# Optimization experiments

Hardware: AMD Instinct MI355X
Metric: run time of the kernel (lower is better)

Reference implementation:

```python
import jax, jax.numpy as jnp
import numpy as np

D_MODEL = 1024
N_HEADS = 16
N_GROUPS = 4
HEAD_DIM = D_MODEL // N_HEADS          # 64
HPG = N_HEADS // N_GROUPS              # heads per group = 4
KV_DIM = N_GROUPS * HEAD_DIM           # 256


def setup_inputs() -> dict:
    key = jax.random.key(0)
    ks = jax.random.split(key, 9)
    B, T = 2, 2048
    s = 0.02
    return {
        "x":  jax.random.normal(ks[0], (B, T, D_MODEL), dtype=jnp.float32),
        "Wq": jax.random.normal(ks[1], (D_MODEL, D_MODEL), dtype=jnp.float32) * s,
        "bq": jnp.zeros((D_MODEL,), dtype=jnp.float32),
        "Wk": jax.random.normal(ks[2], (D_MODEL, KV_DIM), dtype=jnp.float32) * s,
        "bk": jnp.zeros((KV_DIM,), dtype=jnp.float32),
        "Wv": jax.random.normal(ks[3], (D_MODEL, KV_DIM), dtype=jnp.float32) * s,
        "bv": jnp.zeros((KV_DIM,), dtype=jnp.float32),
        "Wo": jax.random.normal(ks[4], (D_MODEL, D_MODEL), dtype=jnp.float32) * s,
        "bo": jnp.zeros((D_MODEL,), dtype=jnp.float32),
    }


def reference(x, Wq, bq, Wk, bk, Wv, bv, Wo, bo):
    B, T, C = x.shape
    q = x @ Wq + bq                                   # [B,T,C]
    k = x @ Wk + bk                                   # [B,T,G*hd]
    v = x @ Wv + bv

    # [B, G, hpg, T, hd] for q; [B, G, T, hd] for k,v (native GQA head sharing,
    # equivalent to repeat_interleave on the group dim in the torch code)
    q = q.reshape(B, T, N_GROUPS, HPG, HEAD_DIM).transpose(0, 2, 3, 1, 4)
    k = k.reshape(B, T, N_GROUPS, HEAD_DIM).transpose(0, 2, 1, 3)
    v = v.reshape(B, T, N_GROUPS, HEAD_DIM).transpose(0, 2, 1, 3)

    scale = 1.0 / jnp.sqrt(jnp.float32(HEAD_DIM))
    attn = jnp.einsum('bghqd,bgkd->bghqk', q, k) * scale   # [B,G,hpg,T,T]

    causal = jnp.tril(jnp.ones((T, T), dtype=bool))        # True = keep
    attn = jnp.where(causal, attn, jnp.float32(-jnp.inf))
    attn = jax.nn.softmax(attn, axis=-1)
    # dropout p=0.1 only in training mode; reference is eval mode (identity)

    out = jnp.einsum('bghqk,bgkd->bghqd', attn, v)         # [B,G,hpg,T,hd]
    out = out.transpose(0, 3, 1, 2, 4).reshape(B, T, C)
    return out @ Wo + bo
```

## Files before the change

kernel.cpp:

```cpp
#include <hip/hip_runtime.h>
#include <hip/hip_bf16.h>
#include <stdint.h>

#define D_MODEL 1024
#define T_LEN   2048
#define BATCH   2
#define N_HEADS 16
#define KV_DIM  256
#define QKV_N   1536
#define M_ROWS  (BATCH * T_LEN)

typedef unsigned short u16;
typedef __bf16 bf16x8 __attribute__((ext_vector_type(8)));
typedef __bf16 bf16x2 __attribute__((ext_vector_type(2)));
typedef float  f32x4  __attribute__((ext_vector_type(4)));

__device__ __forceinline__ u16 f2b(float f) {
    uint32_t u = __builtin_bit_cast(uint32_t, f);
    u += 0x7FFFu + ((u >> 16) & 1u);
    return (u16)(u >> 16);
}

__device__ __forceinline__ uint32_t pk_bf16(float a, float b) {
#if __has_builtin(__builtin_amdgcn_cvt_pk_bf16_f32)
    bf16x2 v = __builtin_amdgcn_cvt_pk_bf16_f32(a, b);
    return __builtin_bit_cast(uint32_t, v);
#else
    return (uint32_t)f2b(a) | ((uint32_t)f2b(b) << 16);
#endif
}

__device__ __forceinline__ void gl_lds16(const void* g, void* l) {
    __builtin_amdgcn_global_load_lds(g, l, 16, 0, 0);
}

__global__ __launch_bounds__(256) void prep(
    const float* __restrict__ x,
    const float* __restrict__ Wq, const float* __restrict__ Wk,
    const float* __restrict__ Wv, const float* __restrict__ Wo,
    u16* __restrict__ xb, u16* __restrict__ WcatT, u16* __restrict__ WoT)
{
    __shared__ u16 tile[32][33];
    int id = blockIdx.x;
    int tid = threadIdx.x;
    if (id < 2048) {
        int i = (id * 256 + tid) * 8;
        float4 a = *(const float4*)&x[i];
        float4 c = *(const float4*)&x[i + 4];
        u16 r[8] = { f2b(a.x), f2b(a.y), f2b(a.z), f2b(a.w),
                     f2b(c.x), f2b(c.y), f2b(c.z), f2b(c.w) };
        *(uint4*)&xb[i] = *(const uint4*)r;
        return;
    }
    int t = id - 2048;
    int bx = t % 80;
    int k0 = (t / 80) * 32;
    const float* src; u16* dst; int N, n0;
    if (bx < 32)       { src = Wq; dst = WcatT;                   N = 1024; n0 = bx * 32; }
    else if (bx < 40)  { src = Wk; dst = WcatT + 1024 * 1024;     N = 256;  n0 = (bx - 32) * 32; }
    else if (bx < 48)  { src = Wv; dst = WcatT + 1280 * 1024;     N = 256;  n0 = (bx - 40) * 32; }
    else               { src = Wo; dst = WoT;                     N = 1024; n0 = (bx - 48) * 32; }
    for (int i = 0; i < 4; ++i) {
        int idx = tid + i * 256;
        int r = idx >> 5, c = idx & 31;
        tile[r][c] = f2b(src[(size_t)(k0 + r) * N + (n0 + c)]);
    }
    __syncthreads();
    for (int i = 0; i < 4; ++i) {
        int idx = tid + i * 256;
        int r = idx >> 5, c = idx & 31;
        dst[(size_t)(n0 + r) * 1024 + (k0 + c)] = tile[c][r];
    }
}

__global__ __launch_bounds__(256) void gemm_qkv(
    const u16* __restrict__ A, const u16* __restrict__ BT,
    const float* __restrict__ bq, const float* __restrict__ bk,
    const float* __restrict__ bv, u16* __restrict__ Qb,
    u16* __restrict__ Kpack, u16* __restrict__ Vpack)
{
    constexpr int K = 1024;
    constexpr float SCALE = 0.125f * 1.44269504088896f;
    __shared__ __align__(16) u16 As[64 * 64];
    __shared__ __align__(16) u16 Bs[128 * 64];

    int tid  = threadIdx.x;
    int lane = tid & 63, w = tid >> 6;
    int quad = lane >> 4, l15 = lane & 15;
    int m0 = blockIdx.y * 64, n0 = blockIdx.x * 128;
    int lr = lane >> 3, lc = (lane & 7) * 8;

    f32x4 acc[4][2] = {};

    for (int k0 = 0; k0 < K; k0 += 64) {
        for (int t = 0; t < 2; ++t) {
            int rb = t * 32 + w * 8;
            gl_lds16(&A[(size_t)(m0 + rb + lr) * K + k0 + lc], &As[rb * 64]);
        }
        for (int t = 0; t < 4; ++t) {
            int rb = t * 32 + w * 8;
            gl_lds16(&BT[(size_t)(n0 + rb + lr) * K + k0 + lc], &Bs[rb * 64]);
        }
        __syncthreads();
        for (int kk = 0; kk < 64; kk += 32) {
            bf16x8 a[4], b[2];
            for (int i = 0; i < 4; ++i)
                a[i] = *(const bf16x8*)&As[(i * 16 + l15) * 64 + kk + quad * 8];
            for (int j = 0; j < 2; ++j)
                b[j] = *(const bf16x8*)&Bs[(w * 32 + j * 16 + l15) * 64 + kk + quad * 8];
            for (int i = 0; i < 4; ++i)
                for (int j = 0; j < 2; ++j)
                    acc[i][j] = __builtin_amdgcn_mfma_f32_16x16x32_bf16(
                        a[i], b[j], acc[i][j], 0, 0, 0);
        }
        __syncthreads();
    }

    for (int j = 0; j < 2; ++j) {
        int col = n0 + w * 32 + j * 16 + l15;
        float bj = (col < 1024) ? bq[col] : (col < 1280) ? bk[col - 1024] : bv[col - 1280];
        for (int i = 0; i < 4; ++i) {
            int rowb = m0 + i * 16 + quad * 4;
            int bb = rowb >> 11, keyloc = rowb & 2047;
            int t64 = keyloc >> 6;
            if (col < 1024) {
                for (int r = 0; r < 4; ++r)
                    Qb[(size_t)(rowb + r) * 1024 + col] =
                        f2b((acc[i][j][r] + bj) * SCALE);
            } else if (col < 1280) {
                int d = col - 1024; int g = d >> 6; d &= 63;
                int kk = d >> 5, qd = (d >> 3) & 3, e = d & 7;
                int ntk = (keyloc >> 4) & 3, l15k = keyloc & 15;
                size_t base = ((((size_t)(bb * 4 + g) * 32 + t64) * 2 + kk) * 4
                               + ntk) * 512 + qd * 128 + l15k * 8 + e;
                for (int r = 0; r < 4; ++r)
                    Kpack[base + r * 8] = f2b(acc[i][j][r] + bj);
            } else {
                int d = col - 1280; int g = d >> 6; d &= 63;
                int dt = d >> 4, l15v = d & 15;
                int kkp = (keyloc >> 5) & 1, qv = (keyloc >> 3) & 3, e0 = keyloc & 7;
                u16 tmp[4];
                for (int r = 0; r < 4; ++r) tmp[r] = f2b(acc[i][j][r] + bj);
                size_t base = ((((size_t)(bb * 4 + g) * 32 + t64) * 2 + kkp) * 4
                               + dt) * 512 + (qv * 16 + l15v) * 8 + e0;
                *(uint64_t*)&Vpack[base] = *(const uint64_t*)tmp;
            }
        }
    }
}

__global__ __launch_bounds__(256) void gemm_out(
    const u16* __restrict__ A, const u16* __restrict__ BT,
    const float* __restrict__ bias, float* __restrict__ C)
{
    constexpr int K = 1024, N = 1024;
    __shared__ __align__(16) u16 As[64 * 64];
    __shared__ __align__(16) u16 Bs[128 * 64];

    int tid  = threadIdx.x;
    int lane = tid & 63, w = tid >> 6;
    int quad = lane >> 4, l15 = lane & 15;
    int m0 = blockIdx.y * 64, n0 = blockIdx.x * 128;
    int lr = lane >> 3, lc = (lane & 7) * 8;

    f32x4 acc[4][2] = {};

    for (int k0 = 0; k0 < K; k0 += 64) {
        for (int t = 0; t < 2; ++t) {
            int rb = t * 32 + w * 8;
            gl_lds16(&A[(size_t)(m0 + rb + lr) * K + k0 + lc], &As[rb * 64]);
        }
        for (int t = 0; t < 4; ++t) {
            int rb = t * 32 + w * 8;
            gl_lds16(&BT[(size_t)(n0 + rb + lr) * K + k0 + lc], &Bs[rb * 64]);
        }
        __syncthreads();
        for (int kk = 0; kk < 64; kk += 32) {
            bf16x8 a[4], b[2];
            for (int i = 0; i < 4; ++i)
                a[i] = *(const bf16x8*)&As[(i * 16 + l15) * 64 + kk + quad * 8];
            for (int j = 0; j < 2; ++j)
                b[j] = *(const bf16x8*)&Bs[(w * 32 + j * 16 + l15) * 64 + kk + quad * 8];
            for (int i = 0; i < 4; ++i)
                for (int j = 0; j < 2; ++j)
                    acc[i][j] = __builtin_amdgcn_mfma_f32_16x16x32_bf16(
                        a[i], b[j], acc[i][j], 0, 0, 0);
        }
        __syncthreads();
    }

    for (int j = 0; j < 2; ++j) {
        int col = n0 + w * 32 + j * 16 + l15;
        float bj = bias[col];
        for (int i = 0; i < 4; ++i) {
            int rowb = m0 + i * 16 + quad * 4;
            for (int r = 0; r < 4; ++r)
                C[(size_t)(rowb + r) * N + col] = acc[i][j][r] + bj;
        }
    }
}

__global__ __launch_bounds__(512, 8) void attn_kernel(
    const u16* __restrict__ Qb,
    const u16* __restrict__ Kpack,
    const u16* __restrict__ Vpack,
    u16* __restrict__ AO)
{
    constexpr int LDP = 72;
    __shared__ __align__(16) u16 Ps[8][16 * LDP];
    __shared__ __align__(16) float Co[4][64][16];
    __shared__ float Cl[4][64];

    int tid  = threadIdx.x;
    int lane = tid & 63, w = tid >> 6;
    int quad = lane >> 4, l15 = lane & 15;
    int hw = w & 3, half = w >> 2;

    int gid = blockIdx.x;
    int b = gid & 1, g = (gid >> 1) & 3;
    int s = gid >> 3;
    int kq = s >> 5, tq = s & 31;
    int q4 = (kq & 1) ? tq : (31 - tq);
    int j  = q4 * 4 + kq;
    int head = g * 4 + hw;
    int q0 = j * 16;
    int iters = q4 + 1;
    int n0 = (iters + 1) >> 1;
    int tgB = half ? n0 : 0;
    int tgE = half ? iters : n0;

    const u16* Qp = Qb + ((size_t)b * T_LEN + q0) * 1024 + head * 64;
    const u16* Kp = Kpack + (size_t)(b * 4 + g) * 131072 + (size_t)lane * 8;
    const u16* Vp = Vpack + (size_t)(b * 4 + g) * 131072 + (size_t)lane * 8;
    u16*       Op = AO + ((size_t)b * T_LEN + q0) * D_MODEL + head * 64;
    u16* Pw = Ps[w];

    bf16x8 Qfrag[2];
    #pragma unroll
    for (int kk = 0; kk < 2; ++kk)
        Qfrag[kk] = *(const bf16x8*)&Qp[(size_t)l15 * 1024 + kk * 32 + quad * 8];

    f32x4 o[4] = {};
    float lsum = 0.f;

    for (int tg = tgB; tg < tgE; ++tg) {
        bool diag = (tg == iters - 1);

        const u16* kb = Kp + (size_t)tg * 4096;
        bf16x8 aK[2][4];
        #pragma unroll
        for (int kk = 0; kk < 2; ++kk)
            #pragma unroll
            for (int ntk = 0; ntk < 4; ++ntk)
                aK[kk][ntk] = *(const bf16x8*)(kb + (kk * 4 + ntk) * 512);

        f32x4 sacc[4] = {};
        #pragma unroll
        for (int kk = 0; kk < 2; ++kk) {
            bf16x8 bQ = Qfrag[kk];
            #pragma unroll
            for (int ntk = 0; ntk < 4; ++ntk)
                sacc[ntk] = __builtin_amdgcn_mfma_f32_16x16x32_bf16(
                    aK[kk][ntk], bQ, sacc[ntk], 0, 0, 0);
        }
        int qrow = q0 + l15;
        float lacc = 0.f;
        #pragma unroll
        for (int ntk = 0; ntk < 4; ++ntk) {
            float p0, p1, p2, p3;
            if (diag) {
                int key = tg * 64 + ntk * 16 + quad * 4;
                p0 = (key + 0 <= qrow) ? exp2f(sacc[ntk][0]) : 0.f;
                p1 = (key + 1 <= qrow) ? exp2f(sacc[ntk][1]) : 0.f;
                p2 = (key + 2 <= qrow) ? exp2f(sacc[ntk][2]) : 0.f;
                p3 = (key + 3 <= qrow) ? exp2f(sacc[ntk][3]) : 0.f;
            } else {
                p0 = exp2f(sacc[ntk][0]);
                p1 = exp2f(sacc[ntk][1]);
                p2 = exp2f(sacc[ntk][2]);
                p3 = exp2f(sacc[ntk][3]);
            }
            lacc += (p0 + p1) + (p2 + p3);
            uint2 pv;
            pv.x = pk_bf16(p0, p1);
            pv.y = pk_bf16(p2, p3);
            *(uint2*)&Pw[l15 * LDP + ntk * 16 + quad * 4] = pv;
        }
        lsum += lacc;

        const u16* vb = Vp + (size_t)tg * 4096;
        #pragma unroll
        for (int kkp = 0; kkp < 2; ++kkp) {
            bf16x8 bV[4];
            #pragma unroll
            for (int dt = 0; dt < 4; ++dt)
                bV[dt] = *(const bf16x8*)(vb + (kkp * 4 + dt) * 512);
            bf16x8 aP = *(const bf16x8*)&Pw[l15 * LDP + kkp * 32 + quad * 8];
            #pragma unroll
            for (int dt = 0; dt < 4; ++dt)
                o[dt] = __builtin_amdgcn_mfma_f32_16x16x32_bf16(
                    aP, bV[dt], o[dt], 0, 0, 0);
        }
    }

    if (half) {
        #pragma unroll
        for (int dt = 0; dt < 4; ++dt)
            *(f32x4*)&Co[hw][lane][dt * 4] = o[dt];
        Cl[hw][lane] = lsum;
    }
    __syncthreads();
    if (!half) {
        #pragma unroll
        for (int dt = 0; dt < 4; ++dt) {
            f32x4 t = *(const f32x4*)&Co[hw][lane][dt * 4];
            o[dt] += t;
        }
        lsum += Cl[hw][lane];

        float l = lsum;
        l += __shfl_xor(l, 16, 64);
        l += __shfl_xor(l, 32, 64);
        float linv = 1.0f / l;
        float li[4];
        #pragma unroll
        for (int r = 0; r < 4; ++r)
            li[r] = __shfl(linv, quad * 4 + r, 64);
        #pragma unroll
        for (int dt = 0; dt < 4; ++dt)
            #pragma unroll
            for (int r = 0; r < 4; ++r)
                Op[(size_t)(quad * 4 + r) * D_MODEL + dt * 16 + l15] =
                    f2b(o[dt][r] * li[r]);
    }
}

extern "C" void kernel_launch(void* const* d_in, const int* in_sizes, int n_in,
                              void* d_out, int out_size, void* d_ws, size_t ws_size,
                              hipStream_t stream) {
    const float* x  = (const float*)d_in[0];
    const float* Wq = (const float*)d_in[1];
    const float* bq = (const float*)d_in[2];
    const float* Wk = (const float*)d_in[3];
    const float* bk = (const float*)d_in[4];
    const float* Wv = (const float*)d_in[5];
    const float* bv = (const float*)d_in[6];
    const float* Wo = (const float*)d_in[7];
    const float* bo = (const float*)d_in[8];
    float* out = (float*)d_out;

    u16* ws    = (u16*)d_ws;
    u16* xb    = ws;  ws += (size_t)M_ROWS * 1024;
    u16* WcatT = ws;  ws += (size_t)QKV_N * 1024;
    u16* WoT   = ws;  ws += 1024 * 1024;
    u16* Qb    = ws;  ws += (size_t)M_ROWS * 1024;
    u16* Kpack = ws;  ws += (size_t)M_ROWS * KV_DIM;
    u16* Vpack = ws;  ws += (size_t)M_ROWS * KV_DIM;
    u16* AO    = xb;

    prep<<<2048 + 2560, 256, 0, stream>>>(x, Wq, Wk, Wv, Wo, xb, WcatT, WoT);
    gemm_qkv<<<dim3(QKV_N / 128, M_ROWS / 64), 256, 0, stream>>>(
        xb, WcatT, bq, bk, bv, Qb, Kpack, Vpack);
    attn_kernel<<<1024, 512, 0, stream>>>(Qb, Kpack, Vpack, AO);
    gemm_out<<<dim3(1024 / 128, M_ROWS / 64), 256, 0, stream>>>(AO, WoT, bo, out);
}
```

Baseline: 203.6 us.

## Switch attention to single-wave blocks with one head and no KV split

The attention kernel now launches 4096 single-wavefront blocks, one per (batch, group, head, 16-row query tile). Each block walks the whole causal key range itself, so the two-half KV split, its LDS combine buffers and the block barrier are gone. Blocks are ordered longest-first to help load balance. The cost is that the four heads of a group no longer share K/V loads inside one block, and the serial loop per wave is up to twice as long.

Result: faster. 188.3 us (-7.5%).

```diff
diff --git a/kernel.cpp b/kernel.cpp
--- a/kernel.cpp
+++ b/kernel.cpp
@@ -200,40 +200,31 @@
     }
 }
 
-__global__ __launch_bounds__(512, 8) void attn_kernel(
+__global__ __launch_bounds__(64, 4) void attn_kernel(
     const u16* __restrict__ Qb,
     const u16* __restrict__ Kpack,
     const u16* __restrict__ Vpack,
     u16* __restrict__ AO)
 {
     constexpr int LDP = 72;
-    __shared__ __align__(16) u16 Ps[8][16 * LDP];
-    __shared__ __align__(16) float Co[4][64][16];
-    __shared__ float Cl[4][64];
-
-    int tid  = threadIdx.x;
-    int lane = tid & 63, w = tid >> 6;
+    __shared__ __align__(16) u16 Pw[16 * LDP];
+
+    int lane = threadIdx.x & 63;
     int quad = lane >> 4, l15 = lane & 15;
-    int hw = w & 3, half = w >> 2;
 
     int gid = blockIdx.x;
     int b = gid & 1, g = (gid >> 1) & 3;
-    int s = gid >> 3;
-    int kq = s >> 5, tq = s & 31;
-    int q4 = (kq & 1) ? tq : (31 - tq);
-    int j  = q4 * 4 + kq;
+    int hw = (gid >> 3) & 3;
+    int s = gid >> 5;
+    int j = 127 - s;
     int head = g * 4 + hw;
     int q0 = j * 16;
-    int iters = q4 + 1;
-    int n0 = (iters + 1) >> 1;
-    int tgB = half ? n0 : 0;
-    int tgE = half ? iters : n0;
+    int iters = (j >> 2) + 1;
 
     const u16* Qp = Qb + ((size_t)b * T_LEN + q0) * 1024 + head * 64;
     const u16* Kp = Kpack + (size_t)(b * 4 + g) * 131072 + (size_t)lane * 8;
     const u16* Vp = Vpack + (size_t)(b * 4 + g) * 131072 + (size_t)lane * 8;
     u16*       Op = AO + ((size_t)b * T_LEN + q0) * D_MODEL + head * 64;
-    u16* Pw = Ps[w];
 
     bf16x8 Qfrag[2];
     #pragma unroll
@@ -243,7 +234,7 @@
     f32x4 o[4] = {};
     float lsum = 0.f;
 
-    for (int tg = tgB; tg < tgE; ++tg) {
+    for (int tg = 0; tg < iters; ++tg) {
         bool diag = (tg == iters - 1);
 
         const u16* kb = Kp + (size_t)tg * 4096;
@@ -303,36 +294,20 @@
         }
     }
 
-    if (half) {
-        #pragma unroll
-        for (int dt = 0; dt < 4; ++dt)
-            *(f32x4*)&Co[hw][lane][dt * 4] = o[dt];
-        Cl[hw][lane] = lsum;
-    }
-    __syncthreads();
-    if (!half) {
-        #pragma unroll
-        for (int dt = 0; dt < 4; ++dt) {
-            f32x4 t = *(const f32x4*)&Co[hw][lane][dt * 4];
-            o[dt] += t;
-        }
-        lsum += Cl[hw][lane];
-
-        float l = lsum;
-        l += __shfl_xor(l, 16, 64);
-        l += __shfl_xor(l, 32, 64);
-        float linv = 1.0f / l;
-        float li[4];
+    float l = lsum;
+    l += __shfl_xor(l, 16, 64);
+    l += __shfl_xor(l, 32, 64);
+    float linv = 1.0f / l;
+    float li[4];
+    #pragma unroll
+    for (int r = 0; r < 4; ++r)
+        li[r] = __shfl(linv, quad * 4 + r, 64);
+    #pragma unroll
+    for (int dt = 0; dt < 4; ++dt)
         #pragma unroll
         for (int r = 0; r < 4; ++r)
-            li[r] = __shfl(linv, quad * 4 + r, 64);
-        #pragma unroll
-        for (int dt = 0; dt < 4; ++dt)
-            #pragma unroll
-            for (int r = 0; r < 4; ++r)
-                Op[(size_t)(quad * 4 + r) * D_MODEL + dt * 16 + l15] =
-                    f2b(o[dt][r] * li[r]);
-    }
+            Op[(size_t)(quad * 4 + r) * D_MODEL + dt * 16 + l15] =
+                f2b(o[dt][r] * li[r]);
 }
 
 extern "C" void kernel_launch(void* const* d_in, const int* in_sizes, int n_in,
@@ -361,6 +336,6 @@
     prep<<<2048 + 2560, 256, 0, stream>>>(x, Wq, Wk, Wv, Wo, xb, WcatT, WoT);
     gemm_qkv<<<dim3(QKV_N / 128, M_ROWS / 64), 256, 0, stream>>>(
         xb, WcatT, bq, bk, bv, Qb, Kpack, Vpack);
-    attn_kernel<<<1024, 512, 0, stream>>>(Qb, Kpack, Vpack, AO);
+    attn_kernel<<<4096, 64, 0, stream>>>(Qb, Kpack, Vpack, AO);
     gemm_out<<<dim3(1024 / 128, M_ROWS / 64), 256, 0, stream>>>(AO, WoT, bo, out);
 }
```
